# Optimization experiments

Hardware: AMD Instinct MI355X
Metric: run time of the kernel (lower is better)

The kernel has to match this reference:

```python
import jax, jax.numpy as jnp
import numpy as np

DIM = 1024
H = 16
HD = DIM // H  # 64
B, N = 2, 2048
EPS = 1e-6


def setup_inputs() -> dict:
    key = jax.random.key(0)
    ks = jax.random.split(key, 12)
    s = 0.02
    return {
        "x": jax.random.normal(ks[0], (B, N, DIM), jnp.float32),
        "rotary_cos": jax.random.uniform(ks[1], (B, N, HD), jnp.float32),
        "rotary_sin": jax.random.uniform(ks[2], (B, N, HD), jnp.float32),
        "Wq": jax.random.normal(ks[3], (DIM, DIM), jnp.float32) * s,
        "bq": jnp.zeros((DIM,), jnp.float32),
        "Wk": jax.random.normal(ks[4], (DIM, DIM), jnp.float32) * s,
        "bk": jnp.zeros((DIM,), jnp.float32),
        "Wv": jax.random.normal(ks[5], (DIM, DIM), jnp.float32) * s,
        "bv": jnp.zeros((DIM,), jnp.float32),
        "q_norm_w": jnp.ones((HD,), jnp.float32),
        "q_norm_b": jnp.zeros((HD,), jnp.float32),
        "k_norm_w": jnp.ones((HD,), jnp.float32),
        "k_norm_b": jnp.zeros((HD,), jnp.float32),
        "Wo": jax.random.normal(ks[6], (DIM, DIM), jnp.float32) * s,
        "bo": jnp.zeros((DIM,), jnp.float32),
    }


def _layernorm(x, w, b):
    mu = jnp.mean(x, axis=-1, keepdims=True)
    var = jnp.mean(jnp.square(x - mu), axis=-1, keepdims=True)
    return (x - mu) * jax.lax.rsqrt(var + EPS) * w + b


def _rotate_half(x):
    x1, x2 = jnp.split(x, 2, axis=-1)
    return jnp.concatenate((-x2, x1), axis=-1)


def _apply_rope(x, cos, sin):
    # x: [B,H,N,D]; cos/sin: [B,N,D] -> [B,1,N,D]
    cos = cos[:, None]
    sin = sin[:, None]
    return x * cos + _rotate_half(x) * sin


def reference(x, rotary_cos, rotary_sin, Wq, bq, Wk, bk, Wv, bv,
              q_norm_w, q_norm_b, k_norm_w, k_norm_b, Wo, bo):
    b, n, c = x.shape
    q = x @ Wq + bq
    k = x @ Wk + bk
    v = x @ Wv + bv
    # Faithful packed-qkv permutation: cat -> view(.., H, 3*hd) -> split(hd)
    qkv = jnp.concatenate((q, k, v), axis=-1).reshape(b, n, H, 3 * HD)
    q, k, v = jnp.split(qkv, 3, axis=-1)  # each [B,N,H,HD]
    q = q.transpose(0, 2, 1, 3)  # [B,H,N,HD]
    k = k.transpose(0, 2, 1, 3)
    v = v.transpose(0, 2, 1, 3)
    q = _layernorm(q, q_norm_w, q_norm_b)
    k = _layernorm(k, k_norm_w, k_norm_b)
    q = _apply_rope(q, rotary_cos, rotary_sin)
    k = _apply_rope(k, rotary_cos, rotary_sin)
    scale = HD ** -0.5
    scores = jnp.einsum("bhqd,bhkd->bhqk", q, k) * scale
    probs = jax.nn.softmax(scores, axis=-1)
    out = jnp.einsum("bhqk,bhkd->bhqd", probs, v)
    out = out.transpose(0, 2, 1, 3).reshape(b, n, c)
    return out @ Wo + bo
```

## Files before the change

### kernel.cpp

```cpp
#include <hip/hip_runtime.h>

typedef __attribute__((ext_vector_type(8))) __bf16 bf16x8;
typedef __attribute__((ext_vector_type(4))) float  f32x4;

#define DEV __device__ __forceinline__

DEV void async_copy16(const void* g, void* l) {
  __builtin_amdgcn_global_load_lds((const __attribute__((address_space(1))) void*)g,
                                   (__attribute__((address_space(3))) void*)l, 16, 0, 0);
}

DEV float ldf(const void* p, size_t i, int isbf) {
  if (isbf) {
    unsigned int w = ((unsigned int)((const unsigned short*)p)[i]) << 16;
    float f; __builtin_memcpy(&f, &w, 4); return f;
  }
  return ((const float*)p)[i];
}

DEV int detect_isbf(const unsigned short* __restrict__ x) {
  int bad = 0;
#pragma unroll
  for (int i = 0; i < 64; i++) {
    int e = (x[i] >> 7) & 0xFF;
    bad |= (e >= 0x90) ? 1 : 0;
  }
  return !bad;
}

__global__ __launch_bounds__(256) void prep(const void* __restrict__ Wq,
                                            const void* __restrict__ Wk,
                                            const void* __restrict__ Wv,
                                            const void* __restrict__ Wo,
                                            const void* __restrict__ x,
                                            const void* __restrict__ bq,
                                            const void* __restrict__ bk,
                                            const void* __restrict__ bv,
                                            const void* __restrict__ bo,
                                            __bf16* __restrict__ Wt,
                                            __bf16* __restrict__ Wot,
                                            __bf16* __restrict__ x_bf,
                                            float* __restrict__ bias) {
  __shared__ float tile[32][33];
  const int isbf = detect_isbf((const unsigned short*)x);
  const int tid = threadIdx.x;
  const int z = blockIdx.z;

  if (z < 4) {
    const void* in = (z == 0) ? Wq : (z == 1) ? Wk : (z == 2) ? Wv : Wo;
    __bf16* out = (z < 3) ? (Wt + (size_t)z * 1024 * 1024) : Wot;
    const int tx = tid & 31, ty = tid >> 5;
    const int r0 = blockIdx.y * 32, c0 = blockIdx.x * 32;
#pragma unroll
    for (int i = 0; i < 4; i++) {
      int r = ty + i * 8;
      tile[r][tx] = ldf(in, (size_t)(r0 + r) * 1024 + c0 + tx, isbf);
    }
    __syncthreads();
#pragma unroll
    for (int i = 0; i < 4; i++) {
      int r = ty + i * 8;
      out[(size_t)(c0 + r) * 1024 + r0 + tx] = (__bf16)tile[tx][r];
    }
  } else {
    const int id = blockIdx.y * 32 + blockIdx.x;
    if (!isbf) {
#pragma unroll
      for (int j = 0; j < 4; j++) {
        int idx = id * 1024 + j * 256 + tid;
        float4 f = ((const float4*)x)[idx];
        union { __bf16 h[4]; uint2 u; } pk;
        pk.h[0] = (__bf16)f.x; pk.h[1] = (__bf16)f.y;
        pk.h[2] = (__bf16)f.z; pk.h[3] = (__bf16)f.w;
        ((uint2*)x_bf)[idx] = pk.u;
      }
    }
    if (id < 16) {
      int i = id * 256 + tid;
      if (i < 1024)      bias[i] = ldf(bq, i, isbf);
      else if (i < 2048) bias[i] = ldf(bk, i - 1024, isbf);
      else if (i < 3072) bias[i] = ldf(bv, i - 2048, isbf);
      else               bias[i] = ldf(bo, i - 3072, isbf);
    }
  }
}

template <int DYN, int NT, int ALT>
__global__ __launch_bounds__(256, 2) void gemm_bt(const __bf16* __restrict__ A,
                                                  const __bf16* __restrict__ Aalt,
                                                  const __bf16* __restrict__ Bt,
                                                  const float* __restrict__ bias,
                                                  void* __restrict__ Cout,
                                                  const unsigned short* __restrict__ xdet,
                                                  int M, int N, int K) {
  constexpr int WN = NT / 2;
  constexpr int JB = WN / 16;
  constexpr int NR = NT / 32;
  __shared__ __align__(16) __bf16 As[128 * 64];
  __shared__ __align__(16) __bf16 Bs[NT * 64];
  const int tid = threadIdx.x;
  const int wid = tid >> 6, lane = tid & 63;
  const int m_blk = blockIdx.x * 128, n_blk = blockIdx.y * NT;
  const int wm = (wid & 1) * 64, wn = (wid >> 1) * WN;
  const int l8 = lane >> 3, l7 = lane & 7;
  const int cc = l7 ^ (l8 & 7);
  const int q4 = lane >> 4, l15 = lane & 15;

  int isbf = 1;
  if (DYN || ALT) isbf = detect_isbf(xdet);
  const __bf16* Ap = (ALT && isbf) ? Aalt : A;

  f32x4 acc[4][JB] = {};

  for (int kb = 0; kb < K; kb += 64) {
    __syncthreads();
#pragma unroll
    for (int i = 0; i < 4; i++) {
      int row = i * 32 + wid * 8 + l8;
      async_copy16(Ap + (size_t)(m_blk + row) * K + kb + cc * 8,
                   As + (i * 32 + wid * 8) * 64);
    }
#pragma unroll
    for (int i = 0; i < NR; i++) {
      int row = i * 32 + wid * 8 + l8;
      async_copy16(Bt + (size_t)(n_blk + row) * K + kb + cc * 8,
                   Bs + (i * 32 + wid * 8) * 64);
    }
    __syncthreads();
#pragma unroll
    for (int k0 = 0; k0 < 64; k0 += 32) {
      bf16x8 a[4], b[JB];
#pragma unroll
      for (int i = 0; i < 4; i++) {
        int ra = wm + i * 16 + l15;
        int ba = ra * 8 + (((k0 >> 3) + q4) ^ (ra & 7));
        a[i] = *(const bf16x8*)&As[ba * 8];
      }
#pragma unroll
      for (int j = 0; j < JB; j++) {
        int rb = wn + j * 16 + l15;
        int bb = rb * 8 + (((k0 >> 3) + q4) ^ (rb & 7));
        b[j] = *(const bf16x8*)&Bs[bb * 8];
      }
#pragma unroll
      for (int i = 0; i < 4; i++)
#pragma unroll
        for (int j = 0; j < JB; j++)
          acc[i][j] = __builtin_amdgcn_mfma_f32_16x16x32_bf16(a[i], b[j], acc[i][j], 0, 0, 0);
    }
  }

  float bcol[JB];
#pragma unroll
  for (int j = 0; j < JB; j++) bcol[j] = bias[n_blk + wn + j * 16 + l15];
#pragma unroll
  for (int i = 0; i < 4; i++)
#pragma unroll
    for (int j = 0; j < JB; j++) {
      int col = n_blk + wn + j * 16 + l15;
#pragma unroll
      for (int r = 0; r < 4; r++) {
        int row = m_blk + wm + i * 16 + q4 * 4 + r;
        float v = acc[i][j][r] + bcol[j];
        size_t idx = (size_t)row * N + col;
        if (DYN && !isbf) ((float*)Cout)[idx] = v;
        else              ((__bf16*)Cout)[idx] = (__bf16)v;
      }
    }
}

__global__ __launch_bounds__(256) void ln_rope_v(const __bf16* __restrict__ qkv,
                                                 const void* __restrict__ rcos,
                                                 const void* __restrict__ rsin,
                                                 const void* __restrict__ qw,
                                                 const void* __restrict__ qb,
                                                 const void* __restrict__ kw,
                                                 const void* __restrict__ kb_,
                                                 const unsigned short* __restrict__ xdet,
                                                 __bf16* __restrict__ Qp,
                                                 __bf16* __restrict__ Kp,
                                                 __bf16* __restrict__ Vt) {
  __shared__ __bf16 vt[64][68];
  const int isbf = detect_isbf(xdet);
  const int tid = threadIdx.x, w = tid >> 6, lane = tid & 63;
  const int bh = blockIdx.y, h = bh & 15, b = bh >> 4;
  const int n0 = blockIdx.x * 64;

  float gq = ldf(qw, lane, isbf), bq_ = ldf(qb, lane, isbf);
  float gk = ldf(kw, lane, isbf), bk_ = ldf(kb_, lane, isbf);

  for (int t = 0; t < 16; t++) {
    const int n = n0 + w * 16 + t;
    const size_t tok = (size_t)b * 2048 + n;
    const __bf16* base = qkv + tok * 3072 + h * 192;
    float qv = (float)base[lane], kv = (float)base[64 + lane], vv = (float)base[128 + lane];

    float sq = qv, sk = kv;
#pragma unroll
    for (int m = 1; m < 64; m <<= 1) { sq += __shfl_xor(sq, m, 64); sk += __shfl_xor(sk, m, 64); }
    float muq = sq * (1.0f / 64.0f), muk = sk * (1.0f / 64.0f);
    float tq = qv - muq, tk = kv - muk;
    float vq = tq * tq, vk = tk * tk;
#pragma unroll
    for (int m = 1; m < 64; m <<= 1) { vq += __shfl_xor(vq, m, 64); vk += __shfl_xor(vk, m, 64); }
    float rsq = rsqrtf(vq * (1.0f / 64.0f) + 1e-6f);
    float rsk = rsqrtf(vk * (1.0f / 64.0f) + 1e-6f);
    float qn = tq * rsq * gq + bq_;
    float kn = tk * rsk * gk + bk_;

    float c = ldf(rcos, tok * 64 + lane, isbf), s = ldf(rsin, tok * 64 + lane, isbf);
    float qpart = __shfl_xor(qn, 32, 64), kpart = __shfl_xor(kn, 32, 64);
    float qrh = (lane < 32) ? -qpart : qpart;
    float krh = (lane < 32) ? -kpart : kpart;

    const size_t oidx = ((size_t)bh * 2048 + n) * 64 + lane;
    Qp[oidx] = (__bf16)((qn * c + qrh * s) * 0.1803368801111204f);
    Kp[oidx] = (__bf16)(kn * c + krh * s);
    vt[lane][w * 16 + t] = (__bf16)vv;
  }
  __syncthreads();
  const int row = tid >> 2, qt = tid & 3;
  size_t gbase = (size_t)bh * 64 * 2048 + (size_t)row * 2048 + n0 + qt * 16;
#pragma unroll
  for (int u = 0; u < 4; u++)
    *(uint2*)&Vt[gbase + u * 4] = *(const uint2*)&vt[row][qt * 16 + u * 4];
}

__global__ __launch_bounds__(256, 2) void attn(const __bf16* __restrict__ Qp,
                                               const __bf16* __restrict__ Kp,
                                               const __bf16* __restrict__ Vt,
                                               __bf16* __restrict__ Obuf) {
  __shared__ __align__(16) __bf16 sK[3][4096];
  __shared__ __align__(16) __bf16 sV[3][4096];
  __shared__ __align__(16) __bf16 sP[4][2048];

  const int tid = threadIdx.x, wid = tid >> 6, lane = tid & 63;
  const int q4 = lane >> 4, l15 = lane & 15;
  const int bh = blockIdx.y;
  const int q0w = blockIdx.x * 128 + wid * 32;
  const __bf16* Qb = Qp + (size_t)bh * 2048 * 64;
  const __bf16* Kb = Kp + (size_t)bh * 2048 * 64;
  const __bf16* Vb = Vt + (size_t)bh * 64 * 2048;
  __bf16* sPw = &sP[wid][0];
  const int pbase = (q4 >> 1) * 128 + l15 * 8 + (q4 & 1) * 4;

#define STAGE(kt, bf)                                                                   \
  do {                                                                                  \
    async_copy16(Kb + (size_t)((kt) + wid * 16 + l15) * 64 + q4 * 8,                    \
                 &sK[bf][(wid * 2 + 0) * 512]);                                         \
    async_copy16(Kb + (size_t)((kt) + wid * 16 + l15) * 64 + 32 + q4 * 8,               \
                 &sK[bf][(wid * 2 + 1) * 512]);                                         \
    async_copy16(Vb + (size_t)(wid * 16 + l15) * 2048 + (kt) + q4 * 8,                  \
                 &sV[bf][(wid * 2 + 0) * 512]);                                         \
    async_copy16(Vb + (size_t)(wid * 16 + l15) * 2048 + (kt) + 32 + q4 * 8,             \
                 &sV[bf][(wid * 2 + 1) * 512]);                                         \
  } while (0)

#pragma unroll
  for (int qs = 0; qs < 2; qs++)
#pragma unroll
    for (int c = 0; c < 2; c++)
      async_copy16(Qb + (size_t)(q0w + qs * 16 + l15) * 64 + c * 32 + q4 * 8,
                   &sPw[(qs * 2 + c) * 512]);
  STAGE(0, 0);
  STAGE(64, 1);
  asm volatile("s_waitcnt vmcnt(8)" ::: "memory");

  bf16x8 qf[2][2];
#pragma unroll
  for (int qs = 0; qs < 2; qs++)
#pragma unroll
    for (int c = 0; c < 2; c++)
      qf[qs][c] = *(const bf16x8*)&sPw[((qs * 2 + c) * 64 + lane) * 8];

  f32x4 o[2][4] = {};
  float lsum[2] = {0.f, 0.f};
  int buf = 0;

  for (int it = 0; it < 32; ++it) {
    if (it < 31) asm volatile("s_waitcnt vmcnt(4)" ::: "memory");
    else         asm volatile("s_waitcnt vmcnt(0)" ::: "memory");
    asm volatile("s_barrier" ::: "memory");
    if (it <= 29) {
      int b2 = buf + 2; if (b2 >= 3) b2 -= 3;
      STAGE((it + 2) * 64, b2);
    }

    f32x4 sc[2][4];
#pragma unroll
    for (int ks = 0; ks < 4; ks++) {
      bf16x8 ak0 = *(const bf16x8*)&sK[buf][((ks * 2 + 0) * 64 + lane) * 8];
      bf16x8 ak1 = *(const bf16x8*)&sK[buf][((ks * 2 + 1) * 64 + lane) * 8];
#pragma unroll
      for (int qs = 0; qs < 2; qs++) {
        f32x4 z = {0.f, 0.f, 0.f, 0.f};
        z = __builtin_amdgcn_mfma_f32_16x16x32_bf16(ak0, qf[qs][0], z, 0, 0, 0);
        z = __builtin_amdgcn_mfma_f32_16x16x32_bf16(ak1, qf[qs][1], z, 0, 0, 0);
        sc[qs][ks] = z;
      }
    }

#pragma unroll
    for (int qs = 0; qs < 2; qs++)
#pragma unroll
      for (int ks = 0; ks < 4; ks++) {
        union { __bf16 h[4]; uint2 u; } pk;
#pragma unroll
        for (int r = 0; r < 4; r++) {
          float p = exp2f(sc[qs][ks][r]);
          lsum[qs] += p;
          pk.h[r] = (__bf16)p;
        }
        *(uint2*)&sPw[(qs * 2 + (ks >> 1)) * 512 + (ks & 1) * 256 + pbase] = pk.u;
      }
    asm volatile("s_waitcnt lgkmcnt(0)" ::: "memory");

    bf16x8 pb[2][2];
#pragma unroll
    for (int qs = 0; qs < 2; qs++)
#pragma unroll
      for (int c = 0; c < 2; c++)
        pb[qs][c] = *(const bf16x8*)&sPw[((qs * 2 + c) * 64 + lane) * 8];
#pragma unroll
    for (int ds = 0; ds < 4; ds++) {
      bf16x8 av0 = *(const bf16x8*)&sV[buf][((ds * 2 + 0) * 64 + lane) * 8];
      bf16x8 av1 = *(const bf16x8*)&sV[buf][((ds * 2 + 1) * 64 + lane) * 8];
#pragma unroll
      for (int qs = 0; qs < 2; qs++) {
        o[qs][ds] = __builtin_amdgcn_mfma_f32_16x16x32_bf16(av0, pb[qs][0], o[qs][ds], 0, 0, 0);
        o[qs][ds] = __builtin_amdgcn_mfma_f32_16x16x32_bf16(av1, pb[qs][1], o[qs][ds], 0, 0, 0);
      }
    }
    buf = (buf == 2) ? 0 : buf + 1;
  }
#undef STAGE

  const int b = bh >> 4, h = bh & 15;
#pragma unroll
  for (int qs = 0; qs < 2; qs++) {
    float l = lsum[qs];
    l += __shfl_xor(l, 16, 64);
    l += __shfl_xor(l, 32, 64);
    float rl = 1.0f / l;
    size_t base = (size_t)(b * 2048 + q0w + qs * 16 + l15) * 1024 + h * 64;
#pragma unroll
    for (int ds = 0; ds < 4; ds++) {
      union { __bf16 h4[4]; uint2 u; } pk;
#pragma unroll
      for (int r = 0; r < 4; r++) pk.h4[r] = (__bf16)(o[qs][ds][r] * rl);
      *(uint2*)&Obuf[base + ds * 16 + q4 * 4] = pk.u;
    }
  }
}

extern "C" void kernel_launch(void* const* d_in, const int* in_sizes, int n_in,
                              void* d_out, int out_size, void* d_ws, size_t ws_size,
                              hipStream_t stream) {
  const void* x   = d_in[0];
  const void* rc  = d_in[1];
  const void* rs  = d_in[2];
  const void* Wq  = d_in[3];
  const void* bq  = d_in[4];
  const void* Wk  = d_in[5];
  const void* bk  = d_in[6];
  const void* Wv  = d_in[7];
  const void* bv  = d_in[8];
  const void* qnw = d_in[9];
  const void* qnb = d_in[10];
  const void* knw = d_in[11];
  const void* knb = d_in[12];
  const void* Wo  = d_in[13];
  const void* bo  = d_in[14];
  const unsigned short* xdet = (const unsigned short*)x;

  char* ws = (char*)d_ws;
  __bf16* qkv  = (__bf16*)ws;
  __bf16* Obuf = (__bf16*)ws;
  __bf16* Qp   = (__bf16*)(ws + 25165824);
  __bf16* Kp   = (__bf16*)(ws + 33554432);
  __bf16* Vt   = (__bf16*)(ws + 41943040);
  __bf16* Wt   = (__bf16*)(ws + 50331648);
  __bf16* Wot  = (__bf16*)(ws + 56623104);
  float*  bias = (float*)(ws + 58720256);
  __bf16* x_bf = (__bf16*)(ws + 58736640);

  prep<<<dim3(32, 32, 5), 256, 0, stream>>>(Wq, Wk, Wv, Wo, x, bq, bk, bv, bo,
                                            Wt, Wot, x_bf, bias);
  gemm_bt<0, 128, 1><<<dim3(32, 24), 256, 0, stream>>>(x_bf, (const __bf16*)x, Wt, bias,
                                                       qkv, xdet, 4096, 3072, 1024);
  ln_rope_v<<<dim3(32, 32), 256, 0, stream>>>(qkv, rc, rs, qnw, qnb, knw, knb, xdet,
                                              Qp, Kp, Vt);
  attn<<<dim3(16, 32), 256, 0, stream>>>(Qp, Kp, Vt, Obuf);
  gemm_bt<1, 64, 0><<<dim3(32, 16), 256, 0, stream>>>(Obuf, nullptr, Wot, bias + 3072,
                                                      d_out, xdet, 4096, 1024, 1024);
}
```

Baseline: 247.1 us.

## Split attention KV range across two blocks and add combine kernel

Attention now splits the 2048-key range into two halves via a third grid dimension, with each block processing 32-key tiles under double buffering and smaller shared memory, which allows higher occupancy (launch bounds 4). Each split writes unnormalized fp32 partial outputs and row sums, and a new combine kernel sums them, normalizes, and writes bf16 output in the layout the output projection expects. The aim is more blocks in flight (1024 vs 512) to fill the GPU better. The cost is extra fp32 traffic of about 32MB plus one more launch, and the pipeline depth drops from triple to double buffering. Since the softmax uses no max subtraction, the partial sums combine exactly.

```diff
diff --git a/kernel.cpp b/kernel.cpp
--- a/kernel.cpp
+++ b/kernel.cpp
@@ -226,84 +226,74 @@
     *(uint2*)&Vt[gbase + u * 4] = *(const uint2*)&vt[row][qt * 16 + u * 4];
 }
 
-__global__ __launch_bounds__(256, 2) void attn(const __bf16* __restrict__ Qp,
+__global__ __launch_bounds__(256, 4) void attn(const __bf16* __restrict__ Qp,
                                                const __bf16* __restrict__ Kp,
                                                const __bf16* __restrict__ Vt,
-                                               __bf16* __restrict__ Obuf) {
-  __shared__ __align__(16) __bf16 sK[3][4096];
-  __shared__ __align__(16) __bf16 sV[3][4096];
-  __shared__ __align__(16) __bf16 sP[4][2048];
+                                               float* __restrict__ O0,
+                                               float* __restrict__ O1,
+                                               float* __restrict__ lpart) {
+  __shared__ __align__(16) __bf16 sK[2][2048];
+  __shared__ __align__(16) __bf16 sV[2][2048];
+  __shared__ __align__(16) __bf16 sP[4][1024];
 
   const int tid = threadIdx.x, wid = tid >> 6, lane = tid & 63;
   const int q4 = lane >> 4, l15 = lane & 15;
-  const int bh = blockIdx.y;
+  const int bh = blockIdx.y, split = blockIdx.z;
   const int q0w = blockIdx.x * 128 + wid * 32;
+  const int kt0 = split * 1024;
   const __bf16* Qb = Qp + (size_t)bh * 2048 * 64;
   const __bf16* Kb = Kp + (size_t)bh * 2048 * 64;
   const __bf16* Vb = Vt + (size_t)bh * 64 * 2048;
+  float* Op = split ? O1 : O0;
   __bf16* sPw = &sP[wid][0];
   const int pbase = (q4 >> 1) * 128 + l15 * 8 + (q4 & 1) * 4;
 
-#define STAGE(kt, bf)                                                                   \
-  do {                                                                                  \
-    async_copy16(Kb + (size_t)((kt) + wid * 16 + l15) * 64 + q4 * 8,                    \
-                 &sK[bf][(wid * 2 + 0) * 512]);                                         \
-    async_copy16(Kb + (size_t)((kt) + wid * 16 + l15) * 64 + 32 + q4 * 8,               \
-                 &sK[bf][(wid * 2 + 1) * 512]);                                         \
-    async_copy16(Vb + (size_t)(wid * 16 + l15) * 2048 + (kt) + q4 * 8,                  \
-                 &sV[bf][(wid * 2 + 0) * 512]);                                         \
-    async_copy16(Vb + (size_t)(wid * 16 + l15) * 2048 + (kt) + 32 + q4 * 8,             \
-                 &sV[bf][(wid * 2 + 1) * 512]);                                         \
-  } while (0)
-
+  bf16x8 qf[2][2];
 #pragma unroll
   for (int qs = 0; qs < 2; qs++)
 #pragma unroll
     for (int c = 0; c < 2; c++)
-      async_copy16(Qb + (size_t)(q0w + qs * 16 + l15) * 64 + c * 32 + q4 * 8,
-                   &sPw[(qs * 2 + c) * 512]);
-  STAGE(0, 0);
-  STAGE(64, 1);
-  asm volatile("s_waitcnt vmcnt(8)" ::: "memory");
-
-  bf16x8 qf[2][2];
-#pragma unroll
-  for (int qs = 0; qs < 2; qs++)
-#pragma unroll
-    for (int c = 0; c < 2; c++)
-      qf[qs][c] = *(const bf16x8*)&sPw[((qs * 2 + c) * 64 + lane) * 8];
+      qf[qs][c] = *(const bf16x8*)&Qb[(size_t)(q0w + qs * 16 + l15) * 64 + c * 32 + q4 * 8];
 
   f32x4 o[2][4] = {};
   float lsum[2] = {0.f, 0.f};
-  int buf = 0;
+
+#define STAGE(kt, bf)                                                                    \
+  do {                                                                                   \
+    async_copy16(Kb + (size_t)((kt) + (wid >> 1) * 16 + l15) * 64 + (wid & 1) * 32 + q4 * 8, \
+                 &sK[bf][wid * 512]);                                                    \
+    async_copy16(Vb + (size_t)(wid * 16 + l15) * 2048 + (kt) + q4 * 8,                   \
+                 &sV[bf][wid * 512]);                                                    \
+  } while (0)
+
+  STAGE(kt0, 0);
 
   for (int it = 0; it < 32; ++it) {
-    if (it < 31) asm volatile("s_waitcnt vmcnt(4)" ::: "memory");
-    else         asm volatile("s_waitcnt vmcnt(0)" ::: "memory");
-    asm volatile("s_barrier" ::: "memory");
-    if (it <= 29) {
-      int b2 = buf + 2; if (b2 >= 3) b2 -= 3;
-      STAGE((it + 2) * 64, b2);
-    }
-
-    f32x4 sc[2][4];
-#pragma unroll
-    for (int ks = 0; ks < 4; ks++) {
-      bf16x8 ak0 = *(const bf16x8*)&sK[buf][((ks * 2 + 0) * 64 + lane) * 8];
-      bf16x8 ak1 = *(const bf16x8*)&sK[buf][((ks * 2 + 1) * 64 + lane) * 8];
-#pragma unroll
-      for (int qs = 0; qs < 2; qs++) {
+    const int buf = it & 1;
+    __syncthreads();
+    if (it < 31) STAGE(kt0 + (it + 1) * 32, buf ^ 1);
+
+    bf16x8 ak[2][2];
+#pragma unroll
+    for (int ks = 0; ks < 2; ks++)
+#pragma unroll
+      for (int c = 0; c < 2; c++)
+        ak[ks][c] = *(const bf16x8*)&sK[buf][((ks * 2 + c) * 64 + lane) * 8];
+    f32x4 sc[2][2];
+#pragma unroll
+    for (int qs = 0; qs < 2; qs++)
+#pragma unroll
+      for (int ks = 0; ks < 2; ks++) {
         f32x4 z = {0.f, 0.f, 0.f, 0.f};
-        z = __builtin_amdgcn_mfma_f32_16x16x32_bf16(ak0, qf[qs][0], z, 0, 0, 0);
-        z = __builtin_amdgcn_mfma_f32_16x16x32_bf16(ak1, qf[qs][1], z, 0, 0, 0);
+        z = __builtin_amdgcn_mfma_f32_16x16x32_bf16(ak[ks][0], qf[qs][0], z, 0, 0, 0);
+        z = __builtin_amdgcn_mfma_f32_16x16x32_bf16(ak[ks][1], qf[qs][1], z, 0, 0, 0);
         sc[qs][ks] = z;
       }
-    }
 
 #pragma unroll
     for (int qs = 0; qs < 2; qs++)
 #pragma unroll
-      for (int ks = 0; ks < 4; ks++) {
+      for (int ks = 0; ks < 2; ks++) {
         union { __bf16 h[4]; uint2 u; } pk;
 #pragma unroll
         for (int r = 0; r < 4; r++) {
@@ -311,46 +301,54 @@
           lsum[qs] += p;
           pk.h[r] = (__bf16)p;
         }
-        *(uint2*)&sPw[(qs * 2 + (ks >> 1)) * 512 + (ks & 1) * 256 + pbase] = pk.u;
+        *(uint2*)&sPw[qs * 512 + ks * 256 + pbase] = pk.u;
       }
     asm volatile("s_waitcnt lgkmcnt(0)" ::: "memory");
 
-    bf16x8 pb[2][2];
+    bf16x8 pb[2];
 #pragma unroll
     for (int qs = 0; qs < 2; qs++)
-#pragma unroll
-      for (int c = 0; c < 2; c++)
-        pb[qs][c] = *(const bf16x8*)&sPw[((qs * 2 + c) * 64 + lane) * 8];
+      pb[qs] = *(const bf16x8*)&sPw[(qs * 64 + lane) * 8];
 #pragma unroll
     for (int ds = 0; ds < 4; ds++) {
-      bf16x8 av0 = *(const bf16x8*)&sV[buf][((ds * 2 + 0) * 64 + lane) * 8];
-      bf16x8 av1 = *(const bf16x8*)&sV[buf][((ds * 2 + 1) * 64 + lane) * 8];
-#pragma unroll
-      for (int qs = 0; qs < 2; qs++) {
-        o[qs][ds] = __builtin_amdgcn_mfma_f32_16x16x32_bf16(av0, pb[qs][0], o[qs][ds], 0, 0, 0);
-        o[qs][ds] = __builtin_amdgcn_mfma_f32_16x16x32_bf16(av1, pb[qs][1], o[qs][ds], 0, 0, 0);
-      }
-    }
-    buf = (buf == 2) ? 0 : buf + 1;
+      bf16x8 av = *(const bf16x8*)&sV[buf][(ds * 64 + lane) * 8];
+#pragma unroll
+      for (int qs = 0; qs < 2; qs++)
+        o[qs][ds] = __builtin_amdgcn_mfma_f32_16x16x32_bf16(av, pb[qs], o[qs][ds], 0, 0, 0);
+    }
   }
 #undef STAGE
 
-  const int b = bh >> 4, h = bh & 15;
 #pragma unroll
   for (int qs = 0; qs < 2; qs++) {
+    const int q = q0w + qs * 16 + l15;
     float l = lsum[qs];
     l += __shfl_xor(l, 16, 64);
     l += __shfl_xor(l, 32, 64);
-    float rl = 1.0f / l;
-    size_t base = (size_t)(b * 2048 + q0w + qs * 16 + l15) * 1024 + h * 64;
-#pragma unroll
-    for (int ds = 0; ds < 4; ds++) {
-      union { __bf16 h4[4]; uint2 u; } pk;
-#pragma unroll
-      for (int r = 0; r < 4; r++) pk.h4[r] = (__bf16)(o[qs][ds][r] * rl);
-      *(uint2*)&Obuf[base + ds * 16 + q4 * 4] = pk.u;
-    }
-  }
+    if (q4 == 0) lpart[(size_t)(split * 32 + bh) * 2048 + q] = l;
+    size_t base = ((size_t)bh * 2048 + q) * 64;
+#pragma unroll
+    for (int ds = 0; ds < 4; ds++)
+      *(f32x4*)&Op[base + ds * 16 + q4 * 4] = o[qs][ds];
+  }
+}
+
+__global__ __launch_bounds__(256) void combine(const float* __restrict__ O0,
+                                               const float* __restrict__ O1,
+                                               const float* __restrict__ lpart,
+                                               __bf16* __restrict__ Obuf) {
+  const int idx = blockIdx.x * 256 + threadIdx.x;
+  const int d4 = idx & 15, q = (idx >> 4) & 2047, bh = idx >> 15;
+  const int b = bh >> 4, h = bh & 15;
+  const size_t po = ((size_t)bh * 2048 + q) * 64 + d4 * 4;
+  f32x4 a = *(const f32x4*)&O0[po];
+  f32x4 c = *(const f32x4*)&O1[po];
+  float l = lpart[(size_t)bh * 2048 + q] + lpart[(size_t)(32 + bh) * 2048 + q];
+  float rl = 1.0f / l;
+  union { __bf16 h4[4]; uint2 u; } pk;
+#pragma unroll
+  for (int r = 0; r < 4; r++) pk.h4[r] = (__bf16)((a[r] + c[r]) * rl);
+  *(uint2*)&Obuf[((size_t)(b * 2048 + q)) * 1024 + h * 64 + d4 * 4] = pk.u;
 }
 
 extern "C" void kernel_launch(void* const* d_in, const int* in_sizes, int n_in,
@@ -375,14 +373,17 @@
 
   char* ws = (char*)d_ws;
   __bf16* qkv  = (__bf16*)ws;
-  __bf16* Obuf = (__bf16*)ws;
-  __bf16* Qp   = (__bf16*)(ws + 25165824);
-  __bf16* Kp   = (__bf16*)(ws + 33554432);
-  __bf16* Vt   = (__bf16*)(ws + 41943040);
-  __bf16* Wt   = (__bf16*)(ws + 50331648);
-  __bf16* Wot  = (__bf16*)(ws + 56623104);
-  float*  bias = (float*)(ws + 58720256);
-  __bf16* x_bf = (__bf16*)(ws + 58736640);
+  float*  O0   = (float*)ws;
+  float*  O1   = (float*)(ws + 16777216);
+  __bf16* x_bf = (__bf16*)(ws + 25165824);
+  __bf16* Qp   = (__bf16*)(ws + 33554432);
+  __bf16* Obuf = (__bf16*)(ws + 33554432);
+  __bf16* Kp   = (__bf16*)(ws + 41943040);
+  __bf16* Vt   = (__bf16*)(ws + 50331648);
+  __bf16* Wt   = (__bf16*)(ws + 58720256);
+  __bf16* Wot  = (__bf16*)(ws + 65011712);
+  float*  bias = (float*)(ws + 67108864);
+  float*  lprt = (float*)(ws + 67125248);
 
   prep<<<dim3(32, 32, 5), 256, 0, stream>>>(Wq, Wk, Wv, Wo, x, bq, bk, bv, bo,
                                             Wt, Wot, x_bf, bias);
@@ -390,7 +391,8 @@
                                                        qkv, xdet, 4096, 3072, 1024);
   ln_rope_v<<<dim3(32, 32), 256, 0, stream>>>(qkv, rc, rs, qnw, qnb, knw, knb, xdet,
                                               Qp, Kp, Vt);
-  attn<<<dim3(16, 32), 256, 0, stream>>>(Qp, Kp, Vt, Obuf);
+  attn<<<dim3(16, 32, 2), 256, 0, stream>>>(Qp, Kp, Vt, O0, O1, lprt);
+  combine<<<4096, 256, 0, stream>>>(O0, O1, lprt, Obuf);
   gemm_bt<1, 64, 0><<<dim3(32, 16), 256, 0, stream>>>(Obuf, nullptr, Wot, bias + 3072,
                                                       d_out, xdet, 4096, 1024, 1024);
 }
```

Measured after the change: 257.5 us. 1.04x slower.
